# Kernel optimization log

Measured on AMD Instinct MI355X. Metric: run time of the kernel, lower is better.

The kernel has to match this reference:

```python
import jax, jax.numpy as jnp
import numpy as np

N = 100_000   # total nodes (batched graph)
E = 1_600_000 # edges (avg degree 16)
W = 100       # window_size (node feature dim)
H = 60        # hidden = ceil(0.6 * window_size)


def setup_inputs() -> dict:
    key = jax.random.key(0)
    ks = jax.random.split(key, 6)
    x = jax.random.normal(ks[0], (N, W), dtype=jnp.float32)
    batch_edge_index = jax.random.randint(ks[1], (2, E), 0, N, dtype=jnp.int32)
    gcn_w = jax.random.normal(ks[2], (W, W), dtype=jnp.float32) * 0.1
    gcn_b = jnp.zeros((W,), dtype=jnp.float32)
    w1 = jax.random.normal(ks[3], (H, W), dtype=jnp.float32) * 0.1
    b1 = jnp.zeros((H,), dtype=jnp.float32)
    w2 = jax.random.normal(ks[4], (W, H), dtype=jnp.float32) * 0.1
    b2 = jnp.zeros((W,), dtype=jnp.float32)
    return {"x": x, "batch_edge_index": batch_edge_index,
            "gcn_w": gcn_w, "gcn_b": gcn_b,
            "w1": w1, "b1": b1, "w2": w2, "b2": b2}


def reference(x, batch_edge_index, gcn_w, gcn_b, w1, b1, w2, b2):
    n = x.shape[0]
    # GCNConv: add self-loops, symmetric normalization D^-1/2 A D^-1/2
    loop = jnp.arange(n, dtype=batch_edge_index.dtype)
    src = jnp.concatenate([batch_edge_index[0], loop])
    dst = jnp.concatenate([batch_edge_index[1], loop])
    deg = jax.ops.segment_sum(jnp.ones(src.shape[0], jnp.float32), dst, num_segments=n)
    dinv = jnp.where(deg > 0, jax.lax.rsqrt(deg), 0.0)
    norm = dinv[src] * dinv[dst]                      # [E+N]
    xw = x @ gcn_w.T                                  # [N, W] linear transform
    msg = xw[src] * norm[:, None]                     # gather + scale
    out = jax.ops.segment_sum(msg, dst, num_segments=n) + gcn_b  # scatter-add
    # relu + tanh MLP head
    h = jax.nn.relu(out)
    h = jnp.tanh(h @ w1.T + b1)
    return jnp.tanh(h @ w2.T + b2)
```

## Files before the change

### kernel.cpp

```cpp
#include <hip/hip_runtime.h>
#include <hip/hip_bf16.h>

#define WDIM 100
#define HDIM 60
#define NPART 8
#define CAP 64

typedef short bf16x8 __attribute__((ext_vector_type(8)));
typedef float f32x4 __attribute__((ext_vector_type(4)));

__device__ inline unsigned short bf_hi_u(float v) {
    return __bfloat16_as_ushort(__float2bfloat16(v));
}
__device__ inline unsigned int pack2(float v0, float v1) {
    return (unsigned int)bf_hi_u(v0) | ((unsigned int)bf_hi_u(v1) << 16);
}

__global__ __launch_bounds__(256) void k_zero(int* __restrict__ cnt, int N) {
    int i = blockIdx.x * blockDim.x + threadIdx.x;
    int stride = gridDim.x * blockDim.x;
    for (int idx = i; idx < N; idx += stride) cnt[idx] = 0;
}

__global__ __launch_bounds__(256) void k_fill(const int* __restrict__ src,
                                              const int* __restrict__ dst,
                                              int* __restrict__ cursor,
                                              int* __restrict__ e_idx, int E, int npp) {
    const int xcd = blockIdx.x & (NPART - 1);
    const int lo = xcd * npp, hi = lo + npp;
    int i = (blockIdx.x >> 3) * blockDim.x + threadIdx.x;
    int stride = (gridDim.x >> 3) * blockDim.x;
    for (int e = i; e < E; e += stride) {
        int d = dst[e];
        if (d >= lo && d < hi) {
            int pos = atomicAdd(&cursor[d], 1);
            if (pos < CAP)
                e_idx[(size_t)d * CAP + pos] = src[e];
        }
    }
}

__global__ __launch_bounds__(256) void k_dinv(const int* __restrict__ cnt,
                                              float* __restrict__ dinv, int N) {
    int i = blockIdx.x * blockDim.x + threadIdx.x;
    int stride = gridDim.x * blockDim.x;
    for (int idx = i; idx < N; idx += stride)
        dinv[idx] = rsqrtf((float)(cnt[idx] + 1));
}

__global__ __launch_bounds__(256) void k_xw(const float* __restrict__ x,
                                            const float* __restrict__ gw,
                                            const float* __restrict__ dinv,
                                            unsigned int* __restrict__ xwh,
                                            int N, int ntiles) {
    __shared__ char wlds[112 * 256];
    const int tid = threadIdx.x;
    for (int w = tid; w < 112 * 64; w += 256) {
        int j = w >> 6, kp = w & 63;
        unsigned int val = 0;
        if (j < 100 && kp < 50)
            val = pack2(gw[j * 100 + 2 * kp], gw[j * 100 + 2 * kp + 1]);
        *(unsigned int*)&wlds[j * 256 + ((kp * 4) ^ ((j & 7) << 4))] = val;
    }
    __syncthreads();

    const int wv = tid >> 6, l = tid & 63;
    const int arow = wv * 16 + (l & 15);
    const int koff = (l >> 4) * 8;
    const int cl = l & 15;
    const int nodeb = wv * 16 + (l >> 4) * 4;

    for (int tile = blockIdx.x; tile < ntiles; tile += gridDim.x) {
        const int n0 = tile * 64;
        int ga = n0 + arow;
        int grow = (ga < N) ? ga : (N - 1);
        const float* __restrict__ xr = x + (size_t)grow * 100;
        bf16x8 ah[4];
#pragma unroll
        for (int kt = 0; kt < 4; ++kt) {
            int c0 = kt * 32 + koff;
            float4 fa = (c0 + 4 <= 100) ? *(const float4*)&xr[c0]
                                        : make_float4(0.f, 0.f, 0.f, 0.f);
            float4 fb = (c0 + 8 <= 100) ? *(const float4*)&xr[c0 + 4]
                                        : make_float4(0.f, 0.f, 0.f, 0.f);
            union { unsigned int u[4]; bf16x8 v; } uu;
            uu.u[0] = pack2(fa.x, fa.y);
            uu.u[1] = pack2(fa.z, fa.w);
            uu.u[2] = pack2(fb.x, fb.y);
            uu.u[3] = pack2(fb.z, fb.w);
            ah[kt] = uu.v;
        }
#pragma unroll
        for (int jt = 0; jt < 7; ++jt) {
            f32x4 acc = {0.f, 0.f, 0.f, 0.f};
#pragma unroll
            for (int kt = 0; kt < 4; ++kt) {
                int brow = jt * 16 + cl;
                int off = brow * 256 + (((kt * 32 + koff) * 2) ^ ((brow & 7) << 4));
                bf16x8 b = *(const bf16x8*)&wlds[off];
                acc = __builtin_amdgcn_mfma_f32_16x16x32_bf16(ah[kt], b, acc, 0, 0, 0);
            }
            int col = jt * 16 + cl;
#pragma unroll
            for (int r = 0; r < 4; ++r) {
                int g = n0 + nodeb + r;
                float di = (g < N) ? dinv[g] : 0.0f;
                float v = acc[r] * di;
                float o = __shfl_xor(v, 1);
                if (!(cl & 1) && col < 100 && g < N)
                    xwh[(size_t)g * 50 + (col >> 1)] = pack2(v, o);
            }
        }
    }
}

__global__ __launch_bounds__(256) void k_gather(const int* __restrict__ e_idx,
                                                const int* __restrict__ cnt,
                                                const unsigned int* __restrict__ xwh,
                                                const float* __restrict__ dinv,
                                                const float* __restrict__ gb,
                                                unsigned int* __restrict__ acch, int N) {
    int wid = (blockIdx.x * blockDim.x + threadIdx.x) >> 6;
    int lane = threadIdx.x & 63;
    if (wid >= N) return;
    int lanec = (lane < 50) ? lane : 0;
    const int* __restrict__ row = e_idx + (size_t)wid * CAP;
    int num = cnt[wid];
    num = (num < CAP) ? num : CAP;
    float a0 = 0.f, a1 = 0.f, b0 = 0.f, b1 = 0.f;
    float c0 = 0.f, c1 = 0.f, d0 = 0.f, d1 = 0.f;
    float e0 = 0.f, e1 = 0.f, f0 = 0.f, f1 = 0.f;
    float g0 = 0.f, g1 = 0.f, h0 = 0.f, h1 = 0.f;
    int k = 0;
    int nn8 = num & ~7;
    if (nn8) {
        unsigned int u0 = xwh[(size_t)row[0] * 50 + lanec];
        unsigned int u1 = xwh[(size_t)row[1] * 50 + lanec];
        unsigned int u2 = xwh[(size_t)row[2] * 50 + lanec];
        unsigned int u3 = xwh[(size_t)row[3] * 50 + lanec];
        unsigned int u4 = xwh[(size_t)row[4] * 50 + lanec];
        unsigned int u5 = xwh[(size_t)row[5] * 50 + lanec];
        unsigned int u6 = xwh[(size_t)row[6] * 50 + lanec];
        unsigned int u7 = xwh[(size_t)row[7] * 50 + lanec];
        for (k = 8; k < nn8; k += 8) {
            unsigned int v0 = xwh[(size_t)row[k + 0] * 50 + lanec];
            unsigned int v1 = xwh[(size_t)row[k + 1] * 50 + lanec];
            unsigned int v2 = xwh[(size_t)row[k + 2] * 50 + lanec];
            unsigned int v3 = xwh[(size_t)row[k + 3] * 50 + lanec];
            unsigned int v4 = xwh[(size_t)row[k + 4] * 50 + lanec];
            unsigned int v5 = xwh[(size_t)row[k + 5] * 50 + lanec];
            unsigned int v6 = xwh[(size_t)row[k + 6] * 50 + lanec];
            unsigned int v7 = xwh[(size_t)row[k + 7] * 50 + lanec];
            a0 += __uint_as_float(u0 << 16); a1 += __uint_as_float(u0 & 0xffff0000u);
            b0 += __uint_as_float(u1 << 16); b1 += __uint_as_float(u1 & 0xffff0000u);
            c0 += __uint_as_float(u2 << 16); c1 += __uint_as_float(u2 & 0xffff0000u);
            d0 += __uint_as_float(u3 << 16); d1 += __uint_as_float(u3 & 0xffff0000u);
            e0 += __uint_as_float(u4 << 16); e1 += __uint_as_float(u4 & 0xffff0000u);
            f0 += __uint_as_float(u5 << 16); f1 += __uint_as_float(u5 & 0xffff0000u);
            g0 += __uint_as_float(u6 << 16); g1 += __uint_as_float(u6 & 0xffff0000u);
            h0 += __uint_as_float(u7 << 16); h1 += __uint_as_float(u7 & 0xffff0000u);
            u0 = v0; u1 = v1; u2 = v2; u3 = v3;
            u4 = v4; u5 = v5; u6 = v6; u7 = v7;
        }
        a0 += __uint_as_float(u0 << 16); a1 += __uint_as_float(u0 & 0xffff0000u);
        b0 += __uint_as_float(u1 << 16); b1 += __uint_as_float(u1 & 0xffff0000u);
        c0 += __uint_as_float(u2 << 16); c1 += __uint_as_float(u2 & 0xffff0000u);
        d0 += __uint_as_float(u3 << 16); d1 += __uint_as_float(u3 & 0xffff0000u);
        e0 += __uint_as_float(u4 << 16); e1 += __uint_as_float(u4 & 0xffff0000u);
        f0 += __uint_as_float(u5 << 16); f1 += __uint_as_float(u5 & 0xffff0000u);
        g0 += __uint_as_float(u6 << 16); g1 += __uint_as_float(u6 & 0xffff0000u);
        h0 += __uint_as_float(u7 << 16); h1 += __uint_as_float(u7 & 0xffff0000u);
        k = nn8;
    }
    for (; k < num; ++k) {
        unsigned int u = xwh[(size_t)row[k] * 50 + lanec];
        a0 += __uint_as_float(u << 16); a1 += __uint_as_float(u & 0xffff0000u);
    }
    unsigned int us = xwh[(size_t)wid * 50 + lanec];
    float s0 = ((a0 + b0) + (c0 + d0)) + ((e0 + f0) + (g0 + h0)) + __uint_as_float(us << 16);
    float s1 = ((a1 + b1) + (c1 + d1)) + ((e1 + f1) + (g1 + h1)) + __uint_as_float(us & 0xffff0000u);
    float di = dinv[wid];
    if (lane < 50) {
        float2 gbv = *(const float2*)(gb + 2 * lane);
        float v0 = fmaxf(fmaf(s0, di, gbv.x), 0.0f);
        float v1 = fmaxf(fmaf(s1, di, gbv.y), 0.0f);
        acch[(size_t)wid * 50 + lane] = pack2(v0, v1);
    }
}

__global__ __launch_bounds__(256) void k_hout(const unsigned int* __restrict__ acch,
                                              const float* __restrict__ w1,
                                              const float* __restrict__ b1,
                                              const float* __restrict__ w2,
                                              const float* __restrict__ b2,
                                              float* __restrict__ out,
                                              int N, int ntiles) {
    __shared__ char w1lds[64 * 256];
    __shared__ char w2lds[112 * 128];
    __shared__ char hlds[64 * 128];
    const int tid = threadIdx.x;

    for (int w = tid; w < 64 * 64; w += 256) {
        int j = w >> 6, kp = w & 63;
        unsigned int val = 0;
        if (j < 60 && kp < 50)
            val = pack2(w1[j * 100 + 2 * kp], w1[j * 100 + 2 * kp + 1]);
        *(unsigned int*)&w1lds[j * 256 + ((kp * 4) ^ ((j & 7) << 4))] = val;
    }
    for (int w = tid; w < 112 * 32; w += 256) {
        int j = w >> 5, kp = w & 31;
        unsigned int val = 0;
        if (j < 100 && kp < 30)
            val = pack2(w2[j * 60 + 2 * kp], w2[j * 60 + 2 * kp + 1]);
        *(unsigned int*)&w2lds[j * 128 + ((kp * 4) ^ ((j & 7) << 4))] = val;
    }
    __syncthreads();

    const int wv = tid >> 6, l = tid & 63;
    const int arow = wv * 16 + (l & 15);
    const int koff = (l >> 4) * 8;
    const int cl = l & 15;
    const int nodeb = wv * 16 + (l >> 4) * 4;

    for (int tile = blockIdx.x; tile < ntiles; tile += gridDim.x) {
        const int n0 = tile * 64;
        int ga = n0 + arow;
        int grow = (ga < N) ? ga : (N - 1);
        const unsigned int* __restrict__ ar = acch + (size_t)grow * 50;
        bf16x8 ah2[4];
#pragma unroll
        for (int kt = 0; kt < 4; ++kt) {
            int c0 = kt * 32 + koff;
            int w0 = c0 >> 1;
            uint4 u = make_uint4(0u, 0u, 0u, 0u);
            if (c0 + 8 <= 100) {
                u = *(const uint4*)&ar[w0];
            } else if (c0 + 4 <= 100) {
                uint2 t = *(const uint2*)&ar[w0];
                u.x = t.x; u.y = t.y;
            }
            union { uint4 q; bf16x8 v; } uu; uu.q = u;
            ah2[kt] = uu.v;
        }
        __syncthreads();

#pragma unroll
        for (int jt = 0; jt < 4; ++jt) {
            f32x4 acc = {0.f, 0.f, 0.f, 0.f};
#pragma unroll
            for (int kt = 0; kt < 4; ++kt) {
                int brow = jt * 16 + cl;
                int off = brow * 256 + (((kt * 32 + koff) * 2) ^ ((brow & 7) << 4));
                bf16x8 b = *(const bf16x8*)&w1lds[off];
                acc = __builtin_amdgcn_mfma_f32_16x16x32_bf16(ah2[kt], b, acc, 0, 0, 0);
            }
            int col = jt * 16 + cl;
            float bias = (col < 60) ? b1[col] : 0.0f;
#pragma unroll
            for (int r = 0; r < 4; ++r) {
                float hv = (col < 60) ? tanhf(acc[r] + bias) : 0.0f;
                int node = nodeb + r;
                *(unsigned short*)&hlds[node * 128 + ((col * 2) ^ ((node & 7) << 4))] = bf_hi_u(hv);
            }
        }
        __syncthreads();

        bf16x8 ah3[2];
#pragma unroll
        for (int kt = 0; kt < 2; ++kt) {
            int off = arow * 128 + (((kt * 32 + koff) * 2) ^ ((arow & 7) << 4));
            ah3[kt] = *(const bf16x8*)&hlds[off];
        }

#pragma unroll
        for (int jt = 0; jt < 7; ++jt) {
            f32x4 acc = {0.f, 0.f, 0.f, 0.f};
#pragma unroll
            for (int kt = 0; kt < 2; ++kt) {
                int brow = jt * 16 + cl;
                int off = brow * 128 + (((kt * 32 + koff) * 2) ^ ((brow & 7) << 4));
                bf16x8 b = *(const bf16x8*)&w2lds[off];
                acc = __builtin_amdgcn_mfma_f32_16x16x32_bf16(ah3[kt], b, acc, 0, 0, 0);
            }
            int col = jt * 16 + cl;
            float bias = (col < 100) ? b2[col] : 0.0f;
#pragma unroll
            for (int r = 0; r < 4; ++r) {
                int g = n0 + nodeb + r;
                if (g < N && col < 100)
                    out[(size_t)g * 100 + col] = tanhf(acc[r] + bias);
            }
        }
    }
}

extern "C" void kernel_launch(void* const* d_in, const int* in_sizes, int n_in,
                              void* d_out, int out_size, void* d_ws, size_t ws_size,
                              hipStream_t stream) {
    const float* x   = (const float*)d_in[0];
    const int*   ei  = (const int*)d_in[1];
    const float* gw  = (const float*)d_in[2];
    const float* gb  = (const float*)d_in[3];
    const float* w1  = (const float*)d_in[4];
    const float* b1  = (const float*)d_in[5];
    const float* w2  = (const float*)d_in[6];
    const float* b2  = (const float*)d_in[7];
    float* out = (float*)d_out;

    const int W = in_sizes[3];
    const int N = in_sizes[0] / W;
    const int E = in_sizes[1] / 2;

    const int* src = ei;
    const int* dst = ei + E;

    unsigned int* xwh  = (unsigned int*)d_ws;
    unsigned int* acch = xwh + (size_t)N * 50;
    int*   e_idx = (int*)(acch + (size_t)N * 50);
    int*   cursor = e_idx + (size_t)N * CAP;
    float* dinv = (float*)(cursor + N);

    const int B = 256;
    const int NT = (N + 63) / 64;
    const int npp = (N + NPART - 1) / NPART;
    auto blocks = [](long long work, int cap) {
        long long b = (work + 255) / 256;
        return (int)(b < cap ? b : cap);
    };

    k_zero<<<blocks(N, 2048), B, 0, stream>>>(cursor, N);
    k_fill<<<4096, B, 0, stream>>>(src, dst, cursor, e_idx, E, npp);
    k_dinv<<<blocks(N, 2048), B, 0, stream>>>(cursor, dinv, N);
    k_xw<<<1280, B, 0, stream>>>(x, gw, dinv, xwh, N, NT);
    k_gather<<<(N * 64 + B - 1) / B, B, 0, stream>>>(e_idx, cursor, xwh, dinv, gb, acch, N);
    k_hout<<<1024, B, 0, stream>>>(acch, w1, b1, w2, b2, out, N, NT);
}
```

Before: 224.4 us.

## Vectorize edge fill, fuse dinv into consumers, use fast tanh, retune grids

The edge-bucketing kernel now reads four dst/src indices per thread with int4 loads, and the tail is handled by a single thread. The separate dinv kernel is removed, and rsqrt(deg+1) is recomputed from the count array inside the xw and gather kernels, saving one launch and one array round trip. tanhf in the MLP head is replaced with an exp-based fast tanh. Grid sizes for fill, xw and hout are also changed. The fast tanh slightly reduces accuracy, and the int4 loads assume the dst pointer is 16-byte aligned (E divisible by 4).

```diff
diff --git a/kernel.cpp b/kernel.cpp
--- a/kernel.cpp
+++ b/kernel.cpp
@@ -14,6 +14,11 @@
 }
 __device__ inline unsigned int pack2(float v0, float v1) {
     return (unsigned int)bf_hi_u(v0) | ((unsigned int)bf_hi_u(v1) << 16);
+}
+__device__ inline float fast_tanh(float x) {
+    float xc = fminf(fmaxf(x, -15.f), 15.f);
+    float t = __expf(2.f * xc);
+    return __fdividef(t - 1.f, t + 1.f);
 }
 
 __global__ __launch_bounds__(256) void k_zero(int* __restrict__ cnt, int N) {
@@ -28,29 +33,45 @@
                                               int* __restrict__ e_idx, int E, int npp) {
     const int xcd = blockIdx.x & (NPART - 1);
     const int lo = xcd * npp, hi = lo + npp;
+    const int4* __restrict__ dst4 = (const int4*)dst;
+    const int4* __restrict__ src4 = (const int4*)src;
+    int E4 = E >> 2;
     int i = (blockIdx.x >> 3) * blockDim.x + threadIdx.x;
     int stride = (gridDim.x >> 3) * blockDim.x;
-    for (int e = i; e < E; e += stride) {
-        int d = dst[e];
-        if (d >= lo && d < hi) {
-            int pos = atomicAdd(&cursor[d], 1);
-            if (pos < CAP)
-                e_idx[(size_t)d * CAP + pos] = src[e];
-        }
-    }
-}
-
-__global__ __launch_bounds__(256) void k_dinv(const int* __restrict__ cnt,
-                                              float* __restrict__ dinv, int N) {
-    int i = blockIdx.x * blockDim.x + threadIdx.x;
-    int stride = gridDim.x * blockDim.x;
-    for (int idx = i; idx < N; idx += stride)
-        dinv[idx] = rsqrtf((float)(cnt[idx] + 1));
+    for (int e = i; e < E4; e += stride) {
+        int4 d = dst4[e];
+        int4 s = src4[e];
+        if (d.x >= lo && d.x < hi) {
+            int p = atomicAdd(&cursor[d.x], 1);
+            if (p < CAP) e_idx[(size_t)d.x * CAP + p] = s.x;
+        }
+        if (d.y >= lo && d.y < hi) {
+            int p = atomicAdd(&cursor[d.y], 1);
+            if (p < CAP) e_idx[(size_t)d.y * CAP + p] = s.y;
+        }
+        if (d.z >= lo && d.z < hi) {
+            int p = atomicAdd(&cursor[d.z], 1);
+            if (p < CAP) e_idx[(size_t)d.z * CAP + p] = s.z;
+        }
+        if (d.w >= lo && d.w < hi) {
+            int p = atomicAdd(&cursor[d.w], 1);
+            if (p < CAP) e_idx[(size_t)d.w * CAP + p] = s.w;
+        }
+    }
+    if (i == 0) {
+        for (int e = E4 << 2; e < E; ++e) {
+            int d = dst[e];
+            if (d >= lo && d < hi) {
+                int p = atomicAdd(&cursor[d], 1);
+                if (p < CAP) e_idx[(size_t)d * CAP + p] = src[e];
+            }
+        }
+    }
 }
 
 __global__ __launch_bounds__(256) void k_xw(const float* __restrict__ x,
                                             const float* __restrict__ gw,
-                                            const float* __restrict__ dinv,
+                                            const int* __restrict__ cnt,
                                             unsigned int* __restrict__ xwh,
                                             int N, int ntiles) {
     __shared__ char wlds[112 * 256];
@@ -90,6 +111,12 @@
             uu.u[3] = pack2(fb.z, fb.w);
             ah[kt] = uu.v;
         }
+        float dir[4];
+#pragma unroll
+        for (int r = 0; r < 4; ++r) {
+            int g = n0 + nodeb + r;
+            dir[r] = (g < N) ? rsqrtf((float)(cnt[g] + 1)) : 0.0f;
+        }
 #pragma unroll
         for (int jt = 0; jt < 7; ++jt) {
             f32x4 acc = {0.f, 0.f, 0.f, 0.f};
@@ -104,8 +131,7 @@
 #pragma unroll
             for (int r = 0; r < 4; ++r) {
                 int g = n0 + nodeb + r;
-                float di = (g < N) ? dinv[g] : 0.0f;
-                float v = acc[r] * di;
+                float v = acc[r] * dir[r];
                 float o = __shfl_xor(v, 1);
                 if (!(cl & 1) && col < 100 && g < N)
                     xwh[(size_t)g * 50 + (col >> 1)] = pack2(v, o);
@@ -117,7 +143,6 @@
 __global__ __launch_bounds__(256) void k_gather(const int* __restrict__ e_idx,
                                                 const int* __restrict__ cnt,
                                                 const unsigned int* __restrict__ xwh,
-                                                const float* __restrict__ dinv,
                                                 const float* __restrict__ gb,
                                                 unsigned int* __restrict__ acch, int N) {
     int wid = (blockIdx.x * blockDim.x + threadIdx.x) >> 6;
@@ -125,8 +150,9 @@
     if (wid >= N) return;
     int lanec = (lane < 50) ? lane : 0;
     const int* __restrict__ row = e_idx + (size_t)wid * CAP;
-    int num = cnt[wid];
-    num = (num < CAP) ? num : CAP;
+    int numraw = cnt[wid];
+    int num = (numraw < CAP) ? numraw : CAP;
+    float di = rsqrtf((float)(numraw + 1));
     float a0 = 0.f, a1 = 0.f, b0 = 0.f, b1 = 0.f;
     float c0 = 0.f, c1 = 0.f, d0 = 0.f, d1 = 0.f;
     float e0 = 0.f, e1 = 0.f, f0 = 0.f, f1 = 0.f;
@@ -179,7 +205,6 @@
     unsigned int us = xwh[(size_t)wid * 50 + lanec];
     float s0 = ((a0 + b0) + (c0 + d0)) + ((e0 + f0) + (g0 + h0)) + __uint_as_float(us << 16);
     float s1 = ((a1 + b1) + (c1 + d1)) + ((e1 + f1) + (g1 + h1)) + __uint_as_float(us & 0xffff0000u);
-    float di = dinv[wid];
     if (lane < 50) {
         float2 gbv = *(const float2*)(gb + 2 * lane);
         float v0 = fmaxf(fmaf(s0, di, gbv.x), 0.0f);
@@ -258,7 +283,7 @@
             float bias = (col < 60) ? b1[col] : 0.0f;
 #pragma unroll
             for (int r = 0; r < 4; ++r) {
-                float hv = (col < 60) ? tanhf(acc[r] + bias) : 0.0f;
+                float hv = (col < 60) ? fast_tanh(acc[r] + bias) : 0.0f;
                 int node = nodeb + r;
                 *(unsigned short*)&hlds[node * 128 + ((col * 2) ^ ((node & 7) << 4))] = bf_hi_u(hv);
             }
@@ -288,7 +313,7 @@
             for (int r = 0; r < 4; ++r) {
                 int g = n0 + nodeb + r;
                 if (g < N && col < 100)
-                    out[(size_t)g * 100 + col] = tanhf(acc[r] + bias);
+                    out[(size_t)g * 100 + col] = fast_tanh(acc[r] + bias);
             }
         }
     }
@@ -318,7 +343,6 @@
     unsigned int* acch = xwh + (size_t)N * 50;
     int*   e_idx = (int*)(acch + (size_t)N * 50);
     int*   cursor = e_idx + (size_t)N * CAP;
-    float* dinv = (float*)(cursor + N);
 
     const int B = 256;
     const int NT = (N + 63) / 64;
@@ -329,9 +353,8 @@
     };
 
     k_zero<<<blocks(N, 2048), B, 0, stream>>>(cursor, N);
-    k_fill<<<4096, B, 0, stream>>>(src, dst, cursor, e_idx, E, npp);
-    k_dinv<<<blocks(N, 2048), B, 0, stream>>>(cursor, dinv, N);
-    k_xw<<<1280, B, 0, stream>>>(x, gw, dinv, xwh, N, NT);
-    k_gather<<<(N * 64 + B - 1) / B, B, 0, stream>>>(e_idx, cursor, xwh, dinv, gb, acch, N);
-    k_hout<<<1024, B, 0, stream>>>(acch, w1, b1, w2, b2, out, N, NT);
-}
+    k_fill<<<8192, B, 0, stream>>>(src, dst, cursor, e_idx, E, npp);
+    k_xw<<<782, B, 0, stream>>>(x, gw, cursor, xwh, N, NT);
+    k_gather<<<(N * 64 + B - 1) / B, B, 0, stream>>>(e_idx, cursor, xwh, gb, acch, N);
+    k_hout<<<782, B, 0, stream>>>(acch, w1, b1, w2, b2, out, N, NT);
+}
```

Result: no change. 222.3 us (-1.0%).
